# Optimization experiments

Hardware: AMD Instinct MI355X
Metric: run time of the kernel (lower is better)

## Reference

```python
import jax, jax.numpy as jnp
import numpy as np

K_SEL = 8        # selection budget K
R_ITER = 1       # fixed-point refinement steps r
LAM = 0.5        # lam
MAX_PROXY = 16   # max_proxy_points
KNN_K = 1        # knn_k = max(1, r)


def knn_stats(x, k):
    # x: [B,N,D] -> [B,N,4] stats of k nearest-neighbor distances (self excluded)
    sq = jnp.sum(x * x, axis=-1)
    d2 = sq[:, :, None] + sq[:, None, :] - 2.0 * jnp.einsum('bnd,bmd->bnm', x, x)
    n = x.shape[1]
    d2 = d2 + jnp.eye(n, dtype=x.dtype) * 1e9  # mask self-distance
    neg_vals, _ = jax.lax.top_k(-d2, k)        # k smallest distances
    d = jnp.sqrt(jnp.maximum(-neg_vals, 0.0))  # [B,N,k]
    return jnp.stack([d.mean(-1), d.min(-1), d.max(-1), d.std(-1)], axis=-1)


def build_structural(x, selection_weights=None, knn_k=KNN_K):
    feats = jnp.concatenate([x, knn_stats(x, knn_k)], axis=-1)
    if selection_weights is not None:
        feats = jnp.concatenate([feats, selection_weights[..., None]], axis=-1)
    return feats


def feature_similarity(f):
    fn = f / (jnp.linalg.norm(f, axis=-1, keepdims=True) + 1e-8)
    return jnp.einsum('bnd,bmd->bnm', fn, fn)


def soft_selector(saliency, similarity, log_temp):
    # SoftSelectorProxy.forward
    temp = jnp.clip(jnp.exp(log_temp), 0.1, 10.0)
    y = jax.nn.sigmoid((saliency / (2.0 * LAM) - 0.5) / temp)

    def rescale(y):
        budget = jnp.clip(y.sum(axis=1, keepdims=True), 1e-6, None)
        return y * jnp.minimum(K_SEL / budget, 1.0)

    y = rescale(y)
    for _ in range(R_ITER):
        overlap = jnp.einsum('bnm,bm->bn', similarity, y)
        y = rescale(y / (1.0 + overlap))
    return y


def setup_inputs() -> dict:
    key = jax.random.key(0)
    ks = jax.random.split(key, 8)
    B, N, D, H = 8, 2048, 32, 64
    K_LIFT, D_MODEL = 16, 256
    ANCHOR = D + 4  # structural_feature_dim(input_dim, include_selection=False)
    s = 0.02
    return {
        'x': jax.random.normal(ks[0], (B, N, D), dtype=jnp.float32),
        'log_temp': jnp.zeros((), dtype=jnp.float32),  # init_temperature=1.0
        'W1': jax.random.normal(ks[1], (D, H), dtype=jnp.float32) * s,
        'b1': jnp.zeros((H,), dtype=jnp.float32),
        'W2': jax.random.normal(ks[2], (H, 1), dtype=jnp.float32) * s,
        'b2': jnp.zeros((1,), dtype=jnp.float32),
        'mu': jnp.zeros((ANCHOR,), dtype=jnp.float32),
        'sigma': jnp.ones((ANCHOR,), dtype=jnp.float32),
        'Wl': jax.random.normal(ks[3], (ANCHOR, K_LIFT), dtype=jnp.float32) * s,
        'bl': jnp.zeros((K_LIFT,), dtype=jnp.float32),
        'Wp': jax.random.normal(ks[4], (K_LIFT, D_MODEL), dtype=jnp.float32) * s,
        'bp': jnp.zeros((D_MODEL,), dtype=jnp.float32),
    }


def reference(x, log_temp, W1, b1, W2, b2, mu, sigma, Wl, bl, Wp, bp):
    # CausalEventModel: per-point MLP saliency head
    h = jax.nn.relu(jnp.einsum('bnd,dh->bnh', x, W1) + b1)
    saliency = (jnp.einsum('bnh,ho->bno', h, W2) + b2)[..., 0]  # [B,N]

    structural = build_structural(x, selection_weights=saliency)
    similarity = feature_similarity(structural)                  # [B,N,N]
    y_star = soft_selector(saliency, similarity, log_temp)       # [B,N]

    dense = build_structural(x, selection_weights=None)          # [B,N,anchor]
    lifted = jnp.tanh(jnp.einsum('bna,ak->bnk', (dense - mu) / sigma, Wl) + bl)

    N = lifted.shape[1]
    K_eff = min(N, MAX_PROXY)
    _, top_idx = jax.lax.top_k(y_star, K_eff)                    # [B,K_eff]
    cloud = jnp.take_along_axis(lifted, top_idx[..., None], axis=1)  # [B,K_eff,k]
    tokens = jnp.einsum('bkc,cd->bkd', cloud, Wp) + bp           # [B,K_eff,d_model]
    return tokens, y_star
```

## Files before the change

### kernel.cpp

```cpp
#include <hip/hip_runtime.h>
#include <math.h>

#define B 8
#define N 2048
#define DIM 32
#define HID 64
#define KLIFT 16
#define DMODEL 256
#define KPROXY 16
#define KSEL 8.0f

typedef float f32x4 __attribute__((ext_vector_type(4)));
typedef short bf16x8 __attribute__((ext_vector_type(8)));

__device__ inline unsigned short f2bf(float f) {
  unsigned u = __float_as_uint(f);
  unsigned r = (u + 0x7FFFu + ((u >> 16) & 1u)) >> 16;
  return (unsigned short)r;
}
__device__ inline float bf2f(unsigned short s) {
  return __uint_as_float(((unsigned)s) << 16);
}
__device__ inline float clip_temp(float lt) {
  return fminf(fmaxf(expf(lt), 0.1f), 10.f);
}

__global__ __launch_bounds__(256) void k_prep(
    const float* __restrict__ x, const float* __restrict__ W1,
    const float* __restrict__ b1, const float* __restrict__ W2,
    const float* __restrict__ b2, const float* __restrict__ logt,
    float* __restrict__ sal, float* __restrict__ sq,
    unsigned short* __restrict__ Xhi, unsigned short* __restrict__ Xlo,
    float* __restrict__ partials1, unsigned* __restrict__ nnd2) {
  __shared__ float sW1[DIM * HID];
  __shared__ float sW2[HID], sb1[HID];
  __shared__ float red[4];
  int t = threadIdx.x;
  int lane = t & 63, wid = t >> 6;
  {
    const float4* s4 = (const float4*)W1;
    float4* d4 = (float4*)sW1;
    for (int i = t; i < DIM * HID / 4; i += 256) d4[i] = s4[i];
    if (t < HID) { sW2[t] = W2[t]; sb1[t] = b1[t]; }
  }
  __syncthreads();
  int p = blockIdx.x * 256 + t;
  nnd2[p] = 0x7F7F7F7Fu;
  float xr[DIM];
  const float4* xp = (const float4*)(x + (size_t)p * DIM);
#pragma unroll
  for (int i = 0; i < DIM / 4; i++) {
    float4 v = xp[i];
    xr[4 * i + 0] = v.x; xr[4 * i + 1] = v.y; xr[4 * i + 2] = v.z; xr[4 * i + 3] = v.w;
  }
  float s = 0.f;
#pragma unroll
  for (int d = 0; d < DIM; d++) s = fmaf(xr[d], xr[d], s);
  sq[p] = s;
  float h[HID];
#pragma unroll
  for (int j = 0; j < HID; j++) h[j] = sb1[j];
  for (int d = 0; d < DIM; d++) {
    float xv = xr[d];
    const float4* wrow = (const float4*)(&sW1[d * HID]);
#pragma unroll
    for (int j4 = 0; j4 < HID / 4; j4++) {
      float4 w = wrow[j4];
      h[4 * j4 + 0] = fmaf(xv, w.x, h[4 * j4 + 0]);
      h[4 * j4 + 1] = fmaf(xv, w.y, h[4 * j4 + 1]);
      h[4 * j4 + 2] = fmaf(xv, w.z, h[4 * j4 + 2]);
      h[4 * j4 + 3] = fmaf(xv, w.w, h[4 * j4 + 3]);
    }
  }
  float acc = b2[0];
#pragma unroll
  for (int j = 0; j < HID; j++) acc = fmaf(fmaxf(h[j], 0.f), sW2[j], acc);
  sal[p] = acc;
  float temp = clip_temp(logt[0]);
  float y0 = 1.f / (1.f + expf(-((acc - 0.5f) / temp)));
  float part = y0;
#pragma unroll
  for (int off = 32; off >= 1; off >>= 1) part += __shfl_xor(part, off);
  if (lane == 0) red[wid] = part;
  __syncthreads();
  if (t == 0) partials1[blockIdx.x] = red[0] + red[1] + red[2] + red[3];
  int bb = p >> 11, n = p & (N - 1);
  int tile = n >> 4, c = n & 15;
  size_t tb = ((size_t)(bb * 128 + tile)) * 64;
#pragma unroll
  for (int g = 0; g < 4; g++) {
    bf16x8 hv, lv;
#pragma unroll
    for (int j = 0; j < 8; j++) {
      float v = xr[g * 8 + j];
      unsigned short hb = f2bf(v);
      hv[j] = (short)hb;
      lv[j] = (short)f2bf(v - bf2f(hb));
    }
    size_t off = (tb + (size_t)g * 16 + c) * 8;
    *(bf16x8*)(Xhi + off) = hv;
    *(bf16x8*)(Xlo + off) = lv;
  }
}

__global__ __launch_bounds__(256) void k_nnd(
    const unsigned short* __restrict__ Xhi, const unsigned short* __restrict__ Xlo,
    const float* __restrict__ sq, unsigned* __restrict__ nnd2) {
  int bid = blockIdx.x;
  int bb = bid >> 7;
  int nch = (bid >> 3) & 15;
  int mo = bid & 7;
  int t = threadIdx.x;
  int w = t >> 6, lane = t & 63;
  int c = lane & 15, g = lane >> 4;
  __shared__ unsigned short ldsH[16 * 512];
  __shared__ unsigned short ldsL[16 * 512];
  __shared__ float ssq[256];
  {
    size_t base = ((size_t)(bb * 128 + mo * 16)) * 512;
    const float4* srcH = (const float4*)(Xhi + base);
    const float4* srcL = (const float4*)(Xlo + base);
    float4* dH = (float4*)ldsH;
    float4* dL = (float4*)ldsL;
    for (int i = t; i < 1024; i += 256) { dH[i] = srcH[i]; dL[i] = srcL[i]; }
    ssq[t] = sq[bb * N + mo * 256 + t];
  }
  int nt0 = nch * 8 + w * 2, nt1 = nt0 + 1;
  bf16x8 ah0 = *(const bf16x8*)(Xhi + (((size_t)(bb * 128 + nt0)) * 64 + lane) * 8);
  bf16x8 al0 = *(const bf16x8*)(Xlo + (((size_t)(bb * 128 + nt0)) * 64 + lane) * 8);
  bf16x8 ah1 = *(const bf16x8*)(Xhi + (((size_t)(bb * 128 + nt1)) * 64 + lane) * 8);
  bf16x8 al1 = *(const bf16x8*)(Xlo + (((size_t)(bb * 128 + nt1)) * 64 + lane) * 8);
  __syncthreads();
  float mn0[4] = {1e30f, 1e30f, 1e30f, 1e30f};
  float mn1[4] = {1e30f, 1e30f, 1e30f, 1e30f};
  for (int tt = 0; tt < 16; tt++) {
    bf16x8 bh = ((const bf16x8*)(ldsH + tt * 512))[lane];
    bf16x8 bl2 = ((const bf16x8*)(ldsL + tt * 512))[lane];
    f32x4 a0 = {0.f, 0.f, 0.f, 0.f};
    f32x4 a1 = {0.f, 0.f, 0.f, 0.f};
    a0 = __builtin_amdgcn_mfma_f32_16x16x32_bf16(ah0, bh, a0, 0, 0, 0);
    a1 = __builtin_amdgcn_mfma_f32_16x16x32_bf16(ah1, bh, a1, 0, 0, 0);
    a0 = __builtin_amdgcn_mfma_f32_16x16x32_bf16(ah0, bl2, a0, 0, 0, 0);
    a1 = __builtin_amdgcn_mfma_f32_16x16x32_bf16(ah1, bl2, a1, 0, 0, 0);
    a0 = __builtin_amdgcn_mfma_f32_16x16x32_bf16(al0, bh, a0, 0, 0, 0);
    a1 = __builtin_amdgcn_mfma_f32_16x16x32_bf16(al1, bh, a1, 0, 0, 0);
    float sm = ssq[tt * 16 + c];
    int mtg = mo * 16 + tt;
    bool d0 = (mtg == nt0), d1 = (mtg == nt1);
#pragma unroll
    for (int r = 0; r < 4; r++) {
      float v0 = fmaf(-2.f, a0[r], sm);
      float v1 = fmaf(-2.f, a1[r], sm);
      if (d0 && c == 4 * g + r) v0 = 1e30f;
      if (d1 && c == 4 * g + r) v1 = 1e30f;
      mn0[r] = fminf(mn0[r], v0);
      mn1[r] = fminf(mn1[r], v1);
    }
  }
#pragma unroll
  for (int off = 1; off <= 8; off <<= 1) {
#pragma unroll
    for (int r = 0; r < 4; r++) {
      mn0[r] = fminf(mn0[r], __shfl_xor(mn0[r], off));
      mn1[r] = fminf(mn1[r], __shfl_xor(mn1[r], off));
    }
  }
  if (c == 0) {
#pragma unroll
    for (int r = 0; r < 4; r++) {
      int n0 = nt0 * 16 + 4 * g + r;
      float v = fmaxf(sq[bb * N + n0] + mn0[r], 0.f);
      atomicMin(&nnd2[bb * N + n0], __float_as_uint(v));
      int n1 = nt1 * 16 + 4 * g + r;
      v = fmaxf(sq[bb * N + n1] + mn1[r], 0.f);
      atomicMin(&nnd2[bb * N + n1], __float_as_uint(v));
    }
  }
}

__global__ __launch_bounds__(256) void k_c1(
    const float* __restrict__ x, const float* __restrict__ sal,
    const float* __restrict__ sq, const unsigned* __restrict__ nnd2,
    const float* __restrict__ logt, const float* __restrict__ partials1,
    float* __restrict__ gpart) {
  int bid = blockIdx.x;
  int bb = bid >> 3, ch = bid & 7;
  int t = threadIdx.x, lane = t & 63, wid = t >> 6;
  __shared__ float xs[256][33];
  __shared__ float cs[256];
  __shared__ float gsh[8][32];
  __shared__ float red32[4], red33[4];
  int n = ch * 256 + t;
  size_t base = (size_t)bb * N + n;
  float temp = clip_temp(logt[0]);
  float b1v = 0.f;
  for (int j = 0; j < 8; j++) b1v += partials1[bb * 8 + j];
  float scale1 = fminf(KSEL / fmaxf(b1v, 1e-6f), 1.f);
  float sv = sal[base];
  float y0 = 1.f / (1.f + expf(-((sv - 0.5f) / temp)));
  float y1 = y0 * scale1;
  float dv = sqrtf(__uint_as_float(nnd2[base]));
  float nrm = sqrtf(sq[base] + 3.f * dv * dv + sv * sv) + 1e-8f;
  float cn = y1 / nrm;
  cs[t] = cn;
  {
    const float4* xsrc = (const float4*)(x + ((size_t)bb * N + ch * 256) * DIM);
    for (int j = t; j < 2048; j += 256) {
      float4 v = xsrc[j];
      int pt = j >> 3, c4 = (j & 7) * 4;
      xs[pt][c4 + 0] = v.x; xs[pt][c4 + 1] = v.y;
      xs[pt][c4 + 2] = v.z; xs[pt][c4 + 3] = v.w;
    }
  }
  float v32 = cn * dv, v33 = cn * sv;
#pragma unroll
  for (int off = 32; off >= 1; off >>= 1) {
    v32 += __shfl_xor(v32, off);
    v33 += __shfl_xor(v33, off);
  }
  if (lane == 0) { red32[wid] = v32; red33[wid] = v33; }
  __syncthreads();
  if (t == 0) {
    gpart[(size_t)(bb * 8 + ch) * 36 + 32] = red32[0] + red32[1] + red32[2] + red32[3];
    gpart[(size_t)(bb * 8 + ch) * 36 + 33] = red33[0] + red33[1] + red33[2] + red33[3];
  }
  int d = t & 31, pg = t >> 5;
  float acc = 0.f;
#pragma unroll
  for (int i = 0; i < 32; i++) acc = fmaf(cs[pg * 32 + i], xs[pg * 32 + i][d], acc);
  gsh[pg][d] = acc;
  __syncthreads();
  if (t < 32) {
    float s = 0.f;
#pragma unroll
    for (int pgi = 0; pgi < 8; pgi++) s += gsh[pgi][t];
    gpart[(size_t)(bb * 8 + ch) * 36 + t] = s;
  }
}

__global__ __launch_bounds__(256) void k_c(
    const float* __restrict__ x, const float* __restrict__ sal,
    const float* __restrict__ sq, const unsigned* __restrict__ nnd2,
    const float* __restrict__ logt, const float* __restrict__ partials1,
    const float* __restrict__ gpart, float* __restrict__ partials2,
    float* __restrict__ ystar) {
  int bid = blockIdx.x;
  int bb = bid >> 3, ch = bid & 7;
  int t = threadIdx.x, lane = t & 63, wid = t >> 6;
  __shared__ float gfin[34];
  __shared__ float s1sh;
  __shared__ float red[4];
  if (t < 34) {
    float s = 0.f;
    for (int j = 0; j < 8; j++) s += gpart[(size_t)(bb * 8 + j) * 36 + t];
    gfin[t] = s;
  }
  if (t == 40) {
    float s = 0.f;
    for (int j = 0; j < 8; j++) s += partials1[bb * 8 + j];
    s1sh = fminf(KSEL / fmaxf(s, 1e-6f), 1.f);
  }
  __syncthreads();
  float scale1 = s1sh;
  int n = ch * 256 + t;
  size_t base = (size_t)bb * N + n;
  float temp = clip_temp(logt[0]);
  float sv = sal[base];
  float y0 = 1.f / (1.f + expf(-((sv - 0.5f) / temp)));
  float y1 = y0 * scale1;
  float dv = sqrtf(__uint_as_float(nnd2[base]));
  float nrm = sqrtf(sq[base] + 3.f * dv * dv + sv * sv) + 1e-8f;
  const float4* p4 = (const float4*)(x + base * DIM);
  float ov = 0.f;
#pragma unroll
  for (int cc = 0; cc < 8; cc++) {
    float4 v = p4[cc];
    ov = fmaf(v.x, gfin[4 * cc + 0], ov);
    ov = fmaf(v.y, gfin[4 * cc + 1], ov);
    ov = fmaf(v.z, gfin[4 * cc + 2], ov);
    ov = fmaf(v.w, gfin[4 * cc + 3], ov);
  }
  ov += 3.f * dv * gfin[32] + sv * gfin[33];
  ov /= nrm;
  float y2 = y1 / (1.f + ov);
  ystar[base] = y2;
  float part = y2;
#pragma unroll
  for (int off = 32; off >= 1; off >>= 1) part += __shfl_xor(part, off);
  if (lane == 0) red[wid] = part;
  __syncthreads();
  if (t == 0) partials2[bb * 8 + ch] = red[0] + red[1] + red[2] + red[3];
}

__global__ __launch_bounds__(512) void k_post(
    const float* __restrict__ x, const unsigned* __restrict__ nnd2,
    const float* __restrict__ partials2, const float* __restrict__ mu,
    const float* __restrict__ sigma, const float* __restrict__ Wl,
    const float* __restrict__ bl, const float* __restrict__ Wp,
    const float* __restrict__ bp, float* __restrict__ tok,
    float* __restrict__ ystar) {
  int b = blockIdx.x, t = threadIdx.x;
  int lane = t & 63, wid = t >> 6;
  __shared__ float yv[N];
  __shared__ float bsh;
  __shared__ float candv[128];
  __shared__ int candi[128];
  __shared__ int tix[KPROXY];
  __shared__ float sz[KPROXY][36];
  if (t == 0) {
    float s = 0.f;
    for (int j = 0; j < 8; j++) s += partials2[b * 8 + j];
    bsh = fminf(KSEL / fmaxf(s, 1e-6f), 1.f);
  }
  __syncthreads();
  float scale2 = bsh;
#pragma unroll
  for (int i = 0; i < 4; i++) {
    int n = t + 512 * i;
    float y = ystar[(size_t)b * N + n] * scale2;
    yv[n] = y;
    ystar[(size_t)b * N + n] = y;
  }
  __syncthreads();
  float lv0 = yv[wid * 256 + lane];        int li0 = wid * 256 + lane;
  float lv1 = yv[wid * 256 + 64 + lane];   int li1 = li0 + 64;
  float lv2 = yv[wid * 256 + 128 + lane];  int li2 = li0 + 128;
  float lv3 = yv[wid * 256 + 192 + lane];  int li3 = li0 + 192;
  for (int r = 0; r < KPROXY; r++) {
    float bv = lv0; int bi = li0;
    if (lv1 > bv) { bv = lv1; bi = li1; }
    if (lv2 > bv) { bv = lv2; bi = li2; }
    if (lv3 > bv) { bv = lv3; bi = li3; }
#pragma unroll
    for (int off = 1; off < 64; off <<= 1) {
      float ovv = __shfl_xor(bv, off);
      int oi = __shfl_xor(bi, off);
      if (ovv > bv || (ovv == bv && oi < bi)) { bv = ovv; bi = oi; }
    }
    if (lane == 0) { candv[wid * 16 + r] = bv; candi[wid * 16 + r] = bi; }
    if (li0 == bi) lv0 = -1e30f;
    if (li1 == bi) lv1 = -1e30f;
    if (li2 == bi) lv2 = -1e30f;
    if (li3 == bi) lv3 = -1e30f;
  }
  __syncthreads();
  if (wid == 0) {
    float cv0 = candv[lane], cv1 = candv[lane + 64];
    int ci0 = candi[lane], ci1 = candi[lane + 64];
    for (int r = 0; r < KPROXY; r++) {
      float bv = cv0; int bi = ci0;
      if (cv1 > bv || (cv1 == bv && ci1 < bi)) { bv = cv1; bi = ci1; }
#pragma unroll
      for (int off = 1; off < 64; off <<= 1) {
        float ovv = __shfl_xor(bv, off);
        int oi = __shfl_xor(bi, off);
        if (ovv > bv || (ovv == bv && oi < bi)) { bv = ovv; bi = oi; }
      }
      if (lane == 0) tix[r] = bi;
      if (ci0 == bi) cv0 = -1e30f;
      if (ci1 == bi) cv1 = -1e30f;
    }
  }
  __syncthreads();
  for (int it = 0; it < 2; it++) {
    int k = wid + 8 * it;
    int srow = tix[k];
    if (lane < 36) {
      float f;
      if (lane < 32) f = x[((size_t)b * N + srow) * DIM + lane];
      else if (lane < 35) f = sqrtf(__uint_as_float(nnd2[b * N + srow]));
      else f = 0.f;
      sz[k][lane] = (f - mu[lane]) / sigma[lane];
    }
    __syncthreads();
    float lf = 0.f;
    if (lane < KLIFT) {
      float a = bl[lane];
#pragma unroll
      for (int d = 0; d < 36; d++) a = fmaf(sz[k][d], Wl[d * KLIFT + lane], a);
      lf = tanhf(a);
    }
    float o0 = bp[lane], o1 = bp[lane + 64], o2 = bp[lane + 128], o3 = bp[lane + 192];
#pragma unroll
    for (int j = 0; j < KLIFT; j++) {
      float lj = __shfl(lf, j);
      const float* wr = Wp + j * DMODEL + lane;
      o0 = fmaf(lj, wr[0], o0);
      o1 = fmaf(lj, wr[64], o1);
      o2 = fmaf(lj, wr[128], o2);
      o3 = fmaf(lj, wr[192], o3);
    }
    float* tp = tok + ((size_t)b * KPROXY + k) * DMODEL + lane;
    tp[0] = o0; tp[64] = o1; tp[128] = o2; tp[192] = o3;
  }
}

extern "C" void kernel_launch(void* const* d_in, const int* in_sizes, int n_in,
                              void* d_out, int out_size, void* d_ws, size_t ws_size,
                              hipStream_t stream) {
  const float* x  = (const float*)d_in[0];
  const float* lt = (const float*)d_in[1];
  const float* W1 = (const float*)d_in[2];
  const float* b1 = (const float*)d_in[3];
  const float* W2 = (const float*)d_in[4];
  const float* b2 = (const float*)d_in[5];
  const float* mu = (const float*)d_in[6];
  const float* sg = (const float*)d_in[7];
  const float* Wl = (const float*)d_in[8];
  const float* bl = (const float*)d_in[9];
  const float* Wp = (const float*)d_in[10];
  const float* bp = (const float*)d_in[11];

  float* tok = (float*)d_out;
  float* ystar = tok + B * KPROXY * DMODEL;

  char* ws = (char*)d_ws;
  float* sal          = (float*)(ws);
  float* sq           = (float*)(ws + 65536);
  unsigned* nnd2      = (unsigned*)(ws + 131072);
  float* partials1    = (float*)(ws + 196608);
  float* gpart        = (float*)(ws + 197120);
  float* partials2    = (float*)(ws + 231424);
  unsigned short* Xhi = (unsigned short*)(ws + 262144);
  unsigned short* Xlo = (unsigned short*)(ws + 262144 + 1048576);

  k_prep<<<B * N / 256, 256, 0, stream>>>(x, W1, b1, W2, b2, lt, sal, sq, Xhi, Xlo, partials1, nnd2);
  k_nnd<<<B * 16 * 8, 256, 0, stream>>>(Xhi, Xlo, sq, nnd2);
  k_c1<<<B * 8, 256, 0, stream>>>(x, sal, sq, nnd2, lt, partials1, gpart);
  k_c<<<B * 8, 256, 0, stream>>>(x, sal, sq, nnd2, lt, partials1, gpart, partials2, ystar);
  k_post<<<B, 512, 0, stream>>>(x, nnd2, partials2, mu, sg, Wl, bl, Wp, bp, tok, ystar);
}
```

Measured before the change: 60.18 us.

## Fuse selector refinement, rescale, top-k and token projection into one per-batch kernel

Merges the three tail kernels (similarity-weighted sum, overlap refinement, top-k plus token projection) into a single 1024-thread block per batch. Cross-chunk partial sums now stay in shared memory instead of global workspace, which removes two launches and their global round-trips. In exchange only 8 blocks run the refinement stage, so parallelism drops from 64 blocks to 8, and x is read directly from global memory rather than staged through LDS.

```diff
diff --git a/kernel.cpp b/kernel.cpp
--- a/kernel.cpp
+++ b/kernel.cpp
@@ -178,178 +178,214 @@
   }
 }
 
-__global__ __launch_bounds__(256) void k_c1(
+__global__ __launch_bounds__(1024) void k_sel3(
     const float* __restrict__ x, const float* __restrict__ sal,
     const float* __restrict__ sq, const unsigned* __restrict__ nnd2,
     const float* __restrict__ logt, const float* __restrict__ partials1,
-    float* __restrict__ gpart) {
-  int bid = blockIdx.x;
-  int bb = bid >> 3, ch = bid & 7;
-  int t = threadIdx.x, lane = t & 63, wid = t >> 6;
-  __shared__ float xs[256][33];
-  __shared__ float cs[256];
-  __shared__ float gsh[8][32];
-  __shared__ float red32[4], red33[4];
-  int n = ch * 256 + t;
-  size_t base = (size_t)bb * N + n;
+    const float* __restrict__ mu, const float* __restrict__ sigma,
+    const float* __restrict__ Wl, const float* __restrict__ bl,
+    const float* __restrict__ Wp, const float* __restrict__ bp,
+    float* __restrict__ tok, float* __restrict__ ystar) {
+  int bb = blockIdx.x, t = threadIdx.x;
+  int lane = t & 63, wid = t >> 6;
+  __shared__ float csf[1024];
+  __shared__ float gshf[4][8][32];
+  __shared__ float red32f[16], red33f[16];
+  __shared__ float gpartS[8][36];
+  __shared__ float gfin[34];
+  __shared__ float red2[32];
+  __shared__ float bsh;
+  __shared__ float yv[N];
+  __shared__ float candv[256];
+  __shared__ int candi[256];
+  __shared__ int tix[KPROXY];
+  __shared__ float sz[KPROXY][36];
+  size_t base = (size_t)bb * N;
   float temp = clip_temp(logt[0]);
   float b1v = 0.f;
   for (int j = 0; j < 8; j++) b1v += partials1[bb * 8 + j];
   float scale1 = fminf(KSEL / fmaxf(b1v, 1e-6f), 1.f);
-  float sv = sal[base];
-  float y0 = 1.f / (1.f + expf(-((sv - 0.5f) / temp)));
-  float y1 = y0 * scale1;
-  float dv = sqrtf(__uint_as_float(nnd2[base]));
-  float nrm = sqrtf(sq[base] + 3.f * dv * dv + sv * sv) + 1e-8f;
-  float cn = y1 / nrm;
-  cs[t] = cn;
-  {
-    const float4* xsrc = (const float4*)(x + ((size_t)bb * N + ch * 256) * DIM);
-    for (int j = t; j < 2048; j += 256) {
-      float4 v = xsrc[j];
-      int pt = j >> 3, c4 = (j & 7) * 4;
-      xs[pt][c4 + 0] = v.x; xs[pt][c4 + 1] = v.y;
-      xs[pt][c4 + 2] = v.z; xs[pt][c4 + 3] = v.w;
-    }
-  }
-  float v32 = cn * dv, v33 = cn * sv;
-#pragma unroll
-  for (int off = 32; off >= 1; off >>= 1) {
-    v32 += __shfl_xor(v32, off);
-    v33 += __shfl_xor(v33, off);
-  }
-  if (lane == 0) { red32[wid] = v32; red33[wid] = v33; }
-  __syncthreads();
-  if (t == 0) {
-    gpart[(size_t)(bb * 8 + ch) * 36 + 32] = red32[0] + red32[1] + red32[2] + red32[3];
-    gpart[(size_t)(bb * 8 + ch) * 36 + 33] = red33[0] + red33[1] + red33[2] + red33[3];
-  }
-  int d = t & 31, pg = t >> 5;
-  float acc = 0.f;
-#pragma unroll
-  for (int i = 0; i < 32; i++) acc = fmaf(cs[pg * 32 + i], xs[pg * 32 + i][d], acc);
-  gsh[pg][d] = acc;
-  __syncthreads();
-  if (t < 32) {
-    float s = 0.f;
-#pragma unroll
-    for (int pgi = 0; pgi < 8; pgi++) s += gsh[pgi][t];
-    gpart[(size_t)(bb * 8 + ch) * 36 + t] = s;
-  }
-}
-
-__global__ __launch_bounds__(256) void k_c(
-    const float* __restrict__ x, const float* __restrict__ sal,
-    const float* __restrict__ sq, const unsigned* __restrict__ nnd2,
-    const float* __restrict__ logt, const float* __restrict__ partials1,
-    const float* __restrict__ gpart, float* __restrict__ partials2,
-    float* __restrict__ ystar) {
-  int bid = blockIdx.x;
-  int bb = bid >> 3, ch = bid & 7;
-  int t = threadIdx.x, lane = t & 63, wid = t >> 6;
-  __shared__ float gfin[34];
-  __shared__ float s1sh;
-  __shared__ float red[4];
+
+  float svA, dvA, nrmA, y1A;
+  {
+    int n = t;
+    float sv = sal[base + n];
+    float y0 = 1.f / (1.f + expf(-((sv - 0.5f) / temp)));
+    float y1 = y0 * scale1;
+    float dv = sqrtf(__uint_as_float(nnd2[base + n]));
+    float nrm = sqrtf(sq[base + n] + 3.f * dv * dv + sv * sv) + 1e-8f;
+    float cn = y1 / nrm;
+    csf[t] = cn;
+    svA = sv; dvA = dv; nrmA = nrm; y1A = y1;
+    float v32 = cn * dv, v33 = cn * sv;
+#pragma unroll
+    for (int off = 32; off >= 1; off >>= 1) {
+      v32 += __shfl_xor(v32, off);
+      v33 += __shfl_xor(v33, off);
+    }
+    if (lane == 0) { red32f[wid] = v32; red33f[wid] = v33; }
+  }
+  __syncthreads();
+  {
+    int ch = t >> 8, pg = (t >> 5) & 7, d = t & 31;
+    const float* xc = x + (base + (size_t)ch * 256 + pg * 32) * DIM + d;
+    float acc = 0.f;
+#pragma unroll
+    for (int i = 0; i < 32; i++) acc = fmaf(csf[ch * 256 + pg * 32 + i], xc[i * DIM], acc);
+    gshf[ch][pg][d] = acc;
+  }
+  __syncthreads();
+  {
+    int ch = t >> 8, tt = t & 255;
+    if (tt < 32) {
+      float s = 0.f;
+#pragma unroll
+      for (int pgi = 0; pgi < 8; pgi++) s += gshf[ch][pgi][tt];
+      gpartS[ch][tt] = s;
+    }
+    if (tt == 0) {
+      gpartS[ch][32] = red32f[4 * ch] + red32f[4 * ch + 1] + red32f[4 * ch + 2] + red32f[4 * ch + 3];
+      gpartS[ch][33] = red33f[4 * ch] + red33f[4 * ch + 1] + red33f[4 * ch + 2] + red33f[4 * ch + 3];
+    }
+  }
+  __syncthreads();
+
+  float svB, dvB, nrmB, y1B;
+  {
+    int n = t + 1024;
+    float sv = sal[base + n];
+    float y0 = 1.f / (1.f + expf(-((sv - 0.5f) / temp)));
+    float y1 = y0 * scale1;
+    float dv = sqrtf(__uint_as_float(nnd2[base + n]));
+    float nrm = sqrtf(sq[base + n] + 3.f * dv * dv + sv * sv) + 1e-8f;
+    float cn = y1 / nrm;
+    csf[t] = cn;
+    svB = sv; dvB = dv; nrmB = nrm; y1B = y1;
+    float v32 = cn * dv, v33 = cn * sv;
+#pragma unroll
+    for (int off = 32; off >= 1; off >>= 1) {
+      v32 += __shfl_xor(v32, off);
+      v33 += __shfl_xor(v33, off);
+    }
+    if (lane == 0) { red32f[wid] = v32; red33f[wid] = v33; }
+  }
+  __syncthreads();
+  {
+    int ch4 = t >> 8, pg = (t >> 5) & 7, d = t & 31;
+    const float* xc = x + (base + 1024 + (size_t)ch4 * 256 + pg * 32) * DIM + d;
+    float acc = 0.f;
+#pragma unroll
+    for (int i = 0; i < 32; i++) acc = fmaf(csf[ch4 * 256 + pg * 32 + i], xc[i * DIM], acc);
+    gshf[ch4][pg][d] = acc;
+  }
+  __syncthreads();
+  {
+    int ch4 = t >> 8, tt = t & 255;
+    if (tt < 32) {
+      float s = 0.f;
+#pragma unroll
+      for (int pgi = 0; pgi < 8; pgi++) s += gshf[ch4][pgi][tt];
+      gpartS[4 + ch4][tt] = s;
+    }
+    if (tt == 0) {
+      gpartS[4 + ch4][32] = red32f[4 * ch4] + red32f[4 * ch4 + 1] + red32f[4 * ch4 + 2] + red32f[4 * ch4 + 3];
+      gpartS[4 + ch4][33] = red33f[4 * ch4] + red33f[4 * ch4 + 1] + red33f[4 * ch4 + 2] + red33f[4 * ch4 + 3];
+    }
+  }
+  __syncthreads();
+
   if (t < 34) {
     float s = 0.f;
-    for (int j = 0; j < 8; j++) s += gpart[(size_t)(bb * 8 + j) * 36 + t];
+    for (int j = 0; j < 8; j++) s += gpartS[j][t];
     gfin[t] = s;
   }
-  if (t == 40) {
-    float s = 0.f;
-    for (int j = 0; j < 8; j++) s += partials1[bb * 8 + j];
-    s1sh = fminf(KSEL / fmaxf(s, 1e-6f), 1.f);
-  }
-  __syncthreads();
-  float scale1 = s1sh;
-  int n = ch * 256 + t;
-  size_t base = (size_t)bb * N + n;
-  float temp = clip_temp(logt[0]);
-  float sv = sal[base];
-  float y0 = 1.f / (1.f + expf(-((sv - 0.5f) / temp)));
-  float y1 = y0 * scale1;
-  float dv = sqrtf(__uint_as_float(nnd2[base]));
-  float nrm = sqrtf(sq[base] + 3.f * dv * dv + sv * sv) + 1e-8f;
-  const float4* p4 = (const float4*)(x + base * DIM);
-  float ov = 0.f;
-#pragma unroll
-  for (int cc = 0; cc < 8; cc++) {
-    float4 v = p4[cc];
-    ov = fmaf(v.x, gfin[4 * cc + 0], ov);
-    ov = fmaf(v.y, gfin[4 * cc + 1], ov);
-    ov = fmaf(v.z, gfin[4 * cc + 2], ov);
-    ov = fmaf(v.w, gfin[4 * cc + 3], ov);
-  }
-  ov += 3.f * dv * gfin[32] + sv * gfin[33];
-  ov /= nrm;
-  float y2 = y1 / (1.f + ov);
-  ystar[base] = y2;
-  float part = y2;
-#pragma unroll
-  for (int off = 32; off >= 1; off >>= 1) part += __shfl_xor(part, off);
-  if (lane == 0) red[wid] = part;
-  __syncthreads();
-  if (t == 0) partials2[bb * 8 + ch] = red[0] + red[1] + red[2] + red[3];
-}
-
-__global__ __launch_bounds__(512) void k_post(
-    const float* __restrict__ x, const unsigned* __restrict__ nnd2,
-    const float* __restrict__ partials2, const float* __restrict__ mu,
-    const float* __restrict__ sigma, const float* __restrict__ Wl,
-    const float* __restrict__ bl, const float* __restrict__ Wp,
-    const float* __restrict__ bp, float* __restrict__ tok,
-    float* __restrict__ ystar) {
-  int b = blockIdx.x, t = threadIdx.x;
-  int lane = t & 63, wid = t >> 6;
-  __shared__ float yv[N];
-  __shared__ float bsh;
-  __shared__ float candv[128];
-  __shared__ int candi[128];
-  __shared__ int tix[KPROXY];
-  __shared__ float sz[KPROXY][36];
+  __syncthreads();
+
+  float y20, y21;
+  {
+    const float4* p4 = (const float4*)(x + (base + t) * DIM);
+    float ov = 0.f;
+#pragma unroll
+    for (int cc = 0; cc < 8; cc++) {
+      float4 v = p4[cc];
+      ov = fmaf(v.x, gfin[4 * cc + 0], ov);
+      ov = fmaf(v.y, gfin[4 * cc + 1], ov);
+      ov = fmaf(v.z, gfin[4 * cc + 2], ov);
+      ov = fmaf(v.w, gfin[4 * cc + 3], ov);
+    }
+    ov += 3.f * dvA * gfin[32] + svA * gfin[33];
+    ov /= nrmA;
+    y20 = y1A / (1.f + ov);
+  }
+  {
+    const float4* p4 = (const float4*)(x + (base + t + 1024) * DIM);
+    float ov = 0.f;
+#pragma unroll
+    for (int cc = 0; cc < 8; cc++) {
+      float4 v = p4[cc];
+      ov = fmaf(v.x, gfin[4 * cc + 0], ov);
+      ov = fmaf(v.y, gfin[4 * cc + 1], ov);
+      ov = fmaf(v.z, gfin[4 * cc + 2], ov);
+      ov = fmaf(v.w, gfin[4 * cc + 3], ov);
+    }
+    ov += 3.f * dvB * gfin[32] + svB * gfin[33];
+    ov /= nrmB;
+    y21 = y1B / (1.f + ov);
+  }
+  {
+    float p0 = y20, p1 = y21;
+#pragma unroll
+    for (int off = 32; off >= 1; off >>= 1) {
+      p0 += __shfl_xor(p0, off);
+      p1 += __shfl_xor(p1, off);
+    }
+    if (lane == 0) { red2[wid] = p0; red2[16 + wid] = p1; }
+  }
+  __syncthreads();
   if (t == 0) {
     float s = 0.f;
-    for (int j = 0; j < 8; j++) s += partials2[b * 8 + j];
+    for (int ch = 0; ch < 8; ch++) {
+      float pch = red2[4 * ch] + red2[4 * ch + 1] + red2[4 * ch + 2] + red2[4 * ch + 3];
+      s += pch;
+    }
     bsh = fminf(KSEL / fmaxf(s, 1e-6f), 1.f);
   }
   __syncthreads();
   float scale2 = bsh;
-#pragma unroll
-  for (int i = 0; i < 4; i++) {
-    int n = t + 512 * i;
-    float y = ystar[(size_t)b * N + n] * scale2;
-    yv[n] = y;
-    ystar[(size_t)b * N + n] = y;
-  }
-  __syncthreads();
-  float lv0 = yv[wid * 256 + lane];        int li0 = wid * 256 + lane;
-  float lv1 = yv[wid * 256 + 64 + lane];   int li1 = li0 + 64;
-  float lv2 = yv[wid * 256 + 128 + lane];  int li2 = li0 + 128;
-  float lv3 = yv[wid * 256 + 192 + lane];  int li3 = li0 + 192;
-  for (int r = 0; r < KPROXY; r++) {
-    float bv = lv0; int bi = li0;
-    if (lv1 > bv) { bv = lv1; bi = li1; }
-    if (lv2 > bv) { bv = lv2; bi = li2; }
-    if (lv3 > bv) { bv = lv3; bi = li3; }
-#pragma unroll
-    for (int off = 1; off < 64; off <<= 1) {
-      float ovv = __shfl_xor(bv, off);
-      int oi = __shfl_xor(bi, off);
-      if (ovv > bv || (ovv == bv && oi < bi)) { bv = ovv; bi = oi; }
-    }
-    if (lane == 0) { candv[wid * 16 + r] = bv; candi[wid * 16 + r] = bi; }
-    if (li0 == bi) lv0 = -1e30f;
-    if (li1 == bi) lv1 = -1e30f;
-    if (li2 == bi) lv2 = -1e30f;
-    if (li3 == bi) lv3 = -1e30f;
+  {
+    float ys0 = y20 * scale2, ys1 = y21 * scale2;
+    yv[t] = ys0; yv[t + 1024] = ys1;
+    ystar[base + t] = ys0; ystar[base + t + 1024] = ys1;
+  }
+  __syncthreads();
+  {
+    float lv0 = yv[wid * 128 + lane];      int li0 = wid * 128 + lane;
+    float lv1 = yv[wid * 128 + 64 + lane]; int li1 = li0 + 64;
+    for (int r = 0; r < KPROXY; r++) {
+      float bv = lv0; int bi = li0;
+      if (lv1 > bv) { bv = lv1; bi = li1; }
+#pragma unroll
+      for (int off = 1; off < 64; off <<= 1) {
+        float ovv = __shfl_xor(bv, off);
+        int oi = __shfl_xor(bi, off);
+        if (ovv > bv || (ovv == bv && oi < bi)) { bv = ovv; bi = oi; }
+      }
+      if (lane == 0) { candv[wid * 16 + r] = bv; candi[wid * 16 + r] = bi; }
+      if (li0 == bi) lv0 = -1e30f;
+      if (li1 == bi) lv1 = -1e30f;
+    }
   }
   __syncthreads();
   if (wid == 0) {
     float cv0 = candv[lane], cv1 = candv[lane + 64];
+    float cv2 = candv[lane + 128], cv3 = candv[lane + 192];
     int ci0 = candi[lane], ci1 = candi[lane + 64];
+    int ci2 = candi[lane + 128], ci3 = candi[lane + 192];
     for (int r = 0; r < KPROXY; r++) {
       float bv = cv0; int bi = ci0;
-      if (cv1 > bv || (cv1 == bv && ci1 < bi)) { bv = cv1; bi = ci1; }
+      if (cv1 > bv) { bv = cv1; bi = ci1; }
+      if (cv2 > bv) { bv = cv2; bi = ci2; }
+      if (cv3 > bv) { bv = cv3; bi = ci3; }
 #pragma unroll
       for (int off = 1; off < 64; off <<= 1) {
         float ovv = __shfl_xor(bv, off);
@@ -359,16 +395,18 @@
       if (lane == 0) tix[r] = bi;
       if (ci0 == bi) cv0 = -1e30f;
       if (ci1 == bi) cv1 = -1e30f;
-    }
-  }
-  __syncthreads();
-  for (int it = 0; it < 2; it++) {
-    int k = wid + 8 * it;
+      if (ci2 == bi) cv2 = -1e30f;
+      if (ci3 == bi) cv3 = -1e30f;
+    }
+  }
+  __syncthreads();
+  {
+    int k = wid;
     int srow = tix[k];
     if (lane < 36) {
       float f;
-      if (lane < 32) f = x[((size_t)b * N + srow) * DIM + lane];
-      else if (lane < 35) f = sqrtf(__uint_as_float(nnd2[b * N + srow]));
+      if (lane < 32) f = x[(base + srow) * DIM + lane];
+      else if (lane < 35) f = sqrtf(__uint_as_float(nnd2[base + srow]));
       else f = 0.f;
       sz[k][lane] = (f - mu[lane]) / sigma[lane];
     }
@@ -390,7 +428,7 @@
       o2 = fmaf(lj, wr[128], o2);
       o3 = fmaf(lj, wr[192], o3);
     }
-    float* tp = tok + ((size_t)b * KPROXY + k) * DMODEL + lane;
+    float* tp = tok + ((size_t)bb * KPROXY + k) * DMODEL + lane;
     tp[0] = o0; tp[64] = o1; tp[128] = o2; tp[192] = o3;
   }
 }
@@ -419,14 +457,10 @@
   float* sq           = (float*)(ws + 65536);
   unsigned* nnd2      = (unsigned*)(ws + 131072);
   float* partials1    = (float*)(ws + 196608);
-  float* gpart        = (float*)(ws + 197120);
-  float* partials2    = (float*)(ws + 231424);
   unsigned short* Xhi = (unsigned short*)(ws + 262144);
   unsigned short* Xlo = (unsigned short*)(ws + 262144 + 1048576);
 
   k_prep<<<B * N / 256, 256, 0, stream>>>(x, W1, b1, W2, b2, lt, sal, sq, Xhi, Xlo, partials1, nnd2);
   k_nnd<<<B * 16 * 8, 256, 0, stream>>>(Xhi, Xlo, sq, nnd2);
-  k_c1<<<B * 8, 256, 0, stream>>>(x, sal, sq, nnd2, lt, partials1, gpart);
-  k_c<<<B * 8, 256, 0, stream>>>(x, sal, sq, nnd2, lt, partials1, gpart, partials2, ystar);
-  k_post<<<B, 512, 0, stream>>>(x, nnd2, partials2, mu, sg, Wl, bl, Wp, bp, tok, ystar);
-}
+  k_sel3<<<B, 1024, 0, stream>>>(x, sal, sq, nnd2, lt, partials1, mu, sg, Wl, bl, Wp, bp, tok, ystar);
+}
```

Result: slower. 64.20 us (+6.7%).

## Replace per-batch serial top-k with rank-counting selection and separate token kernel

Applied to the files above, without the earlier changes.

The single-block-per-batch post kernel, which ran 16 rounds of wave-wide argmax reductions, is replaced by a kernel launched with 8 blocks per batch. In it each thread computes the rank of its element by counting larger values across all 2048 entries held in shared memory, and writes its index into a top-16 slot when the rank is below 16. A separate kernel then builds the tokens with one block per selected point. This spreads the selection and token work across many more blocks to cut the latency of the serial tail, at the cost of an O(N^2) comparison pass, an extra launch, and a scratch buffer for y2.

```diff
diff --git a/kernel.cpp b/kernel.cpp
--- a/kernel.cpp
+++ b/kernel.cpp
@@ -243,7 +243,7 @@
     const float* __restrict__ sq, const unsigned* __restrict__ nnd2,
     const float* __restrict__ logt, const float* __restrict__ partials1,
     const float* __restrict__ gpart, float* __restrict__ partials2,
-    float* __restrict__ ystar) {
+    float* __restrict__ y2buf) {
   int bid = blockIdx.x;
   int bb = bid >> 3, ch = bid & 7;
   int t = threadIdx.x, lane = t & 63, wid = t >> 6;
@@ -283,7 +283,7 @@
   ov += 3.f * dv * gfin[32] + sv * gfin[33];
   ov /= nrm;
   float y2 = y1 / (1.f + ov);
-  ystar[base] = y2;
+  y2buf[base] = y2;
   float part = y2;
 #pragma unroll
   for (int off = 32; off >= 1; off >>= 1) part += __shfl_xor(part, off);
@@ -292,107 +292,80 @@
   if (t == 0) partials2[bb * 8 + ch] = red[0] + red[1] + red[2] + red[3];
 }
 
-__global__ __launch_bounds__(512) void k_post(
+__global__ __launch_bounds__(256) void k_post(
+    const float* __restrict__ y2buf, const float* __restrict__ partials2,
+    float* __restrict__ ystar, int* __restrict__ topidx) {
+  int bid = blockIdx.x;
+  int bb = bid >> 3, ch = bid & 7;
+  int t = threadIdx.x;
+  __shared__ float yv[N];
+  __shared__ float s2sh;
+  if (t == 0) {
+    float s = 0.f;
+    for (int j = 0; j < 8; j++) s += partials2[bb * 8 + j];
+    s2sh = fminf(KSEL / fmaxf(s, 1e-6f), 1.f);
+  }
+  __syncthreads();
+  float scale2 = s2sh;
+  {
+    const float4* src = (const float4*)(y2buf + (size_t)bb * N);
+    float4* dst = (float4*)yv;
+#pragma unroll
+    for (int i = 0; i < 2; i++) {
+      float4 v = src[t + 256 * i];
+      v.x *= scale2; v.y *= scale2; v.z *= scale2; v.w *= scale2;
+      dst[t + 256 * i] = v;
+    }
+  }
+  __syncthreads();
+  int n = ch * 256 + t;
+  float vi = yv[n];
+  ystar[(size_t)bb * N + n] = vi;
+  int cnt = 0;
+  const float4* yv4 = (const float4*)yv;
+  for (int j4 = 0; j4 < N / 4; j4++) {
+    float4 v = yv4[j4];
+    int j = j4 * 4;
+    cnt += (v.x > vi || (v.x == vi && (j + 0) < n));
+    cnt += (v.y > vi || (v.y == vi && (j + 1) < n));
+    cnt += (v.z > vi || (v.z == vi && (j + 2) < n));
+    cnt += (v.w > vi || (v.w == vi && (j + 3) < n));
+  }
+  if (cnt < KPROXY) topidx[bb * KPROXY + cnt] = n;
+}
+
+__global__ __launch_bounds__(256) void k_tok(
     const float* __restrict__ x, const unsigned* __restrict__ nnd2,
-    const float* __restrict__ partials2, const float* __restrict__ mu,
+    const int* __restrict__ topidx, const float* __restrict__ mu,
     const float* __restrict__ sigma, const float* __restrict__ Wl,
     const float* __restrict__ bl, const float* __restrict__ Wp,
-    const float* __restrict__ bp, float* __restrict__ tok,
-    float* __restrict__ ystar) {
-  int b = blockIdx.x, t = threadIdx.x;
-  int lane = t & 63, wid = t >> 6;
-  __shared__ float yv[N];
-  __shared__ float bsh;
-  __shared__ float candv[128];
-  __shared__ int candi[128];
-  __shared__ int tix[KPROXY];
-  __shared__ float sz[KPROXY][36];
-  if (t == 0) {
-    float s = 0.f;
-    for (int j = 0; j < 8; j++) s += partials2[b * 8 + j];
-    bsh = fminf(KSEL / fmaxf(s, 1e-6f), 1.f);
-  }
-  __syncthreads();
-  float scale2 = bsh;
-#pragma unroll
-  for (int i = 0; i < 4; i++) {
-    int n = t + 512 * i;
-    float y = ystar[(size_t)b * N + n] * scale2;
-    yv[n] = y;
-    ystar[(size_t)b * N + n] = y;
-  }
-  __syncthreads();
-  float lv0 = yv[wid * 256 + lane];        int li0 = wid * 256 + lane;
-  float lv1 = yv[wid * 256 + 64 + lane];   int li1 = li0 + 64;
-  float lv2 = yv[wid * 256 + 128 + lane];  int li2 = li0 + 128;
-  float lv3 = yv[wid * 256 + 192 + lane];  int li3 = li0 + 192;
-  for (int r = 0; r < KPROXY; r++) {
-    float bv = lv0; int bi = li0;
-    if (lv1 > bv) { bv = lv1; bi = li1; }
-    if (lv2 > bv) { bv = lv2; bi = li2; }
-    if (lv3 > bv) { bv = lv3; bi = li3; }
-#pragma unroll
-    for (int off = 1; off < 64; off <<= 1) {
-      float ovv = __shfl_xor(bv, off);
-      int oi = __shfl_xor(bi, off);
-      if (ovv > bv || (ovv == bv && oi < bi)) { bv = ovv; bi = oi; }
-    }
-    if (lane == 0) { candv[wid * 16 + r] = bv; candi[wid * 16 + r] = bi; }
-    if (li0 == bi) lv0 = -1e30f;
-    if (li1 == bi) lv1 = -1e30f;
-    if (li2 == bi) lv2 = -1e30f;
-    if (li3 == bi) lv3 = -1e30f;
-  }
-  __syncthreads();
-  if (wid == 0) {
-    float cv0 = candv[lane], cv1 = candv[lane + 64];
-    int ci0 = candi[lane], ci1 = candi[lane + 64];
-    for (int r = 0; r < KPROXY; r++) {
-      float bv = cv0; int bi = ci0;
-      if (cv1 > bv || (cv1 == bv && ci1 < bi)) { bv = cv1; bi = ci1; }
-#pragma unroll
-      for (int off = 1; off < 64; off <<= 1) {
-        float ovv = __shfl_xor(bv, off);
-        int oi = __shfl_xor(bi, off);
-        if (ovv > bv || (ovv == bv && oi < bi)) { bv = ovv; bi = oi; }
-      }
-      if (lane == 0) tix[r] = bi;
-      if (ci0 == bi) cv0 = -1e30f;
-      if (ci1 == bi) cv1 = -1e30f;
-    }
-  }
-  __syncthreads();
-  for (int it = 0; it < 2; it++) {
-    int k = wid + 8 * it;
-    int srow = tix[k];
-    if (lane < 36) {
-      float f;
-      if (lane < 32) f = x[((size_t)b * N + srow) * DIM + lane];
-      else if (lane < 35) f = sqrtf(__uint_as_float(nnd2[b * N + srow]));
-      else f = 0.f;
-      sz[k][lane] = (f - mu[lane]) / sigma[lane];
-    }
-    __syncthreads();
-    float lf = 0.f;
-    if (lane < KLIFT) {
-      float a = bl[lane];
-#pragma unroll
-      for (int d = 0; d < 36; d++) a = fmaf(sz[k][d], Wl[d * KLIFT + lane], a);
-      lf = tanhf(a);
-    }
-    float o0 = bp[lane], o1 = bp[lane + 64], o2 = bp[lane + 128], o3 = bp[lane + 192];
-#pragma unroll
-    for (int j = 0; j < KLIFT; j++) {
-      float lj = __shfl(lf, j);
-      const float* wr = Wp + j * DMODEL + lane;
-      o0 = fmaf(lj, wr[0], o0);
-      o1 = fmaf(lj, wr[64], o1);
-      o2 = fmaf(lj, wr[128], o2);
-      o3 = fmaf(lj, wr[192], o3);
-    }
-    float* tp = tok + ((size_t)b * KPROXY + k) * DMODEL + lane;
-    tp[0] = o0; tp[64] = o1; tp[128] = o2; tp[192] = o3;
-  }
+    const float* __restrict__ bp, float* __restrict__ tok) {
+  int bk = blockIdx.x;
+  int b = bk >> 4, k = bk & 15;
+  int t = threadIdx.x;
+  __shared__ float z[36]; __shared__ float lift[KLIFT]; __shared__ int srow;
+  if (t == 0) srow = topidx[b * KPROXY + k];
+  __syncthreads();
+  int n = srow;
+  if (t < 36) {
+    float dvv;
+    if (t < DIM) dvv = x[((size_t)(b * N + n)) * DIM + t];
+    else if (t < 35) dvv = sqrtf(__uint_as_float(nnd2[b * N + n]));
+    else dvv = 0.f;
+    z[t] = (dvv - mu[t]) / sigma[t];
+  }
+  __syncthreads();
+  if (t < KLIFT) {
+    float a = bl[t];
+#pragma unroll
+    for (int d = 0; d < 36; d++) a = fmaf(z[d], Wl[d * KLIFT + t], a);
+    lift[t] = tanhf(a);
+  }
+  __syncthreads();
+  float a = bp[t];
+#pragma unroll
+  for (int j = 0; j < KLIFT; j++) a = fmaf(lift[j], Wp[j * DMODEL + t], a);
+  tok[(size_t)(b * KPROXY + k) * DMODEL + t] = a;
 }
 
 extern "C" void kernel_launch(void* const* d_in, const int* in_sizes, int n_in,
@@ -418,15 +391,18 @@
   float* sal          = (float*)(ws);
   float* sq           = (float*)(ws + 65536);
   unsigned* nnd2      = (unsigned*)(ws + 131072);
-  float* partials1    = (float*)(ws + 196608);
-  float* gpart        = (float*)(ws + 197120);
-  float* partials2    = (float*)(ws + 231424);
-  unsigned short* Xhi = (unsigned short*)(ws + 262144);
-  unsigned short* Xlo = (unsigned short*)(ws + 262144 + 1048576);
+  float* y2buf        = (float*)(ws + 196608);
+  float* partials1    = (float*)(ws + 262144);
+  float* gpart        = (float*)(ws + 262656);
+  float* partials2    = (float*)(ws + 272384);
+  int* topidx         = (int*)(ws + 272896);
+  unsigned short* Xhi = (unsigned short*)(ws + 327680);
+  unsigned short* Xlo = (unsigned short*)(ws + 327680 + 1048576);
 
   k_prep<<<B * N / 256, 256, 0, stream>>>(x, W1, b1, W2, b2, lt, sal, sq, Xhi, Xlo, partials1, nnd2);
   k_nnd<<<B * 16 * 8, 256, 0, stream>>>(Xhi, Xlo, sq, nnd2);
   k_c1<<<B * 8, 256, 0, stream>>>(x, sal, sq, nnd2, lt, partials1, gpart);
-  k_c<<<B * 8, 256, 0, stream>>>(x, sal, sq, nnd2, lt, partials1, gpart, partials2, ystar);
-  k_post<<<B, 512, 0, stream>>>(x, nnd2, partials2, mu, sg, Wl, bl, Wp, bp, tok, ystar);
-}
+  k_c<<<B * 8, 256, 0, stream>>>(x, sal, sq, nnd2, lt, partials1, gpart, partials2, y2buf);
+  k_post<<<B * 8, 256, 0, stream>>>(y2buf, partials2, ystar, topidx);
+  k_tok<<<B * KPROXY, 256, 0, stream>>>(x, nnd2, topidx, mu, sg, Wl, bl, Wp, bp, tok);
+}
```

Result: slower. 89.34 us (+48.4%).
